# Optimization experiments

Hardware: AMD Instinct MI355X
Metric: run time of the kernel (lower is better)

## Reference

```python
import jax, jax.numpy as jnp
import numpy as np

VEC_DIM = 128   # D (also the per-head dim in this module)
HEADS = 8
PATCH = 4
WIN = 7
N_BATCH = 4
H_IMG = 448
W_IMG = 448


def _relative_index():
    # Swin-style relative position index, computed statically (matches torch code
    # which uses torch.meshgrid with default 'ij' indexing).
    coords = np.stack(np.meshgrid(np.arange(WIN), np.arange(WIN), indexing='ij'))  # [2,W,W]
    flat = coords.reshape(2, -1)                      # [2, W*W]
    rel = flat[:, :, None] - flat[:, None, :]         # [2, p, p]
    rel = rel.transpose(1, 2, 0).astype(np.int64)     # [p, p, 2]
    rel[:, :, 0] += WIN - 1
    rel[:, :, 1] += WIN - 1
    rel[:, :, 1] *= 2 * WIN - 1
    return rel.sum(-1)                                # [p, p], values in [0, (2W-1)^2)

REL_IDX = jnp.asarray(_relative_index())


def setup_inputs() -> dict:
    key = jax.random.key(0)
    ks = jax.random.split(key, 8)
    P = (H_IMG // PATCH) * (W_IMG // PATCH)  # 12544
    D, H = VEC_DIM, HEADS
    s = 0.02
    return {
        'x': jax.random.normal(ks[0], (N_BATCH, D, P), jnp.float32),
        'Wq': jax.random.normal(ks[1], (H * D, D), jnp.float32) * s,
        'bq': jnp.zeros((H * D,), jnp.float32),
        'Wk': jax.random.normal(ks[2], (H * D, D), jnp.float32) * s,
        'bk': jnp.zeros((H * D,), jnp.float32),
        'Wv': jax.random.normal(ks[3], (H * D, D), jnp.float32) * s,
        'bv': jnp.zeros((H * D,), jnp.float32),
        'Wo': jax.random.normal(ks[4], (D, H * D), jnp.float32) * s,
        'bo': jnp.zeros((D,), jnp.float32),
        'pos_code': jax.random.normal(ks[5], ((2 * WIN - 1) ** 2, H), jnp.float32) * s,
        'h': H_IMG,
        'w': W_IMG,
    }


def reference(x, Wq, bq, Wk, bk, Wv, bv, Wo, bo, pos_code, h, w):
    N, D, P = x.shape
    H = HEADS
    ch, cw = h // PATCH, w // PATCH
    nh, nw = ch // WIN, cw // WIN            # windows per axis
    p = WIN * WIN                            # tokens per window

    def emb(W, b):
        # pointwise Conv1d: [N,D,P] -> [N,H*D,P] -> [N,H,D,P]
        return (jnp.einsum('od,ndp->nop', W, x) + b[None, :, None]).reshape(N, H, D, P)

    def partition(e):
        # [N,H,D,P] -> [N,H,win_num,D,p]
        e = e.reshape(N, H, D, nh, WIN, nw, WIN)
        return e.transpose(0, 1, 3, 5, 2, 4, 6).reshape(N, H, nh * nw, D, p)

    q = partition(emb(Wq, bq))
    k = partition(emb(Wk, bk))
    v = partition(emb(Wv, bv))

    # attn[n,h,w,i,j] = sum_d k[n,h,w,d,i] * q[n,h,w,d,j], scaled
    attn = jnp.einsum('nhwdi,nhwdj->nhwij', k, q) / (D ** 0.5)
    bias = pos_code[REL_IDX].transpose(2, 0, 1)          # [H, p, p]
    attn = attn + bias[None, :, None, :, :]
    weights = jax.nn.softmax(attn, axis=3)               # softmax over key index i

    # out[n,h,w,d,j] = sum_i v[n,h,w,d,i] * weights[n,h,w,i,j]
    out = jnp.einsum('nhwdi,nhwij->nhwdj', v, weights)

    # window merge: [N,H,win_num,D,p] -> [N,H*D,P]
    out = out.reshape(N, H, nh, nw, D, WIN, WIN)
    out = out.transpose(0, 1, 4, 2, 5, 3, 6).reshape(N, H * D, P)

    return jnp.einsum('od,ndp->nop', Wo, out) + bo[None, :, None]
```

## Files before the change

### kernel.cpp

```cpp
#include <hip/hip_runtime.h>

typedef unsigned short u16;
typedef unsigned int u32;
typedef __attribute__((ext_vector_type(8))) short bf16x8;
typedef __attribute__((ext_vector_type(4))) float f32x4;
typedef __attribute__((ext_vector_type(2))) unsigned int u32x2;

#define NBATCH 4
#define DDIM   128
#define NHEAD  8
#define PTOT   12544
#define CWID   112
#define NTOK   49
#define PSTR   68

#define OFF_TS 0
#define OFF_US 6272
#define OFF_PL 14464
#define OFF_PC 17796
#define OFF_MF 19148
#define OFF_CS 21196
#define LDS_TOT 22220

#define WS_WC   131072
#define WS_F32  262144

__device__ __forceinline__ int swz128(int row, int col) {
    return row * 128 + ((((col >> 3) ^ row) & 15) << 3) + (col & 7);
}
__device__ __forceinline__ int swz64(int row, int col) {
    return row * 64 + ((((col >> 3) ^ row) & 7) << 3) + (col & 7);
}
__device__ __forceinline__ float bf2f(u16 u) {
    union { u32 i; float f; } x; x.i = ((u32)u) << 16; return x.f;
}
__device__ __forceinline__ u16 f2bf(float f) {
    union { float f; u32 u; } v; v.f = f;
    return (u16)((v.u + 0x7fffu + ((v.u >> 16) & 1u)) >> 16);
}

__global__ void __launch_bounds__(256) prep(
    const float* __restrict__ Wq, const float* __restrict__ Wk,
    const float* __restrict__ Wv, const float* __restrict__ Wo,
    const float* __restrict__ bq, const float* __restrict__ bk,
    const float* __restrict__ bv, u16* __restrict__ ws)
{
    __shared__ u16 lm[32768];
    const int tid = threadIdx.x;
    const int b = blockIdx.x;
    const bool isG = (b >= 8);
    const int h = b & 7;
    float* fb = (float*)(ws + WS_F32);

    if (!isG) {
        for (int idx = tid; idx < 16384; idx += 256) {
            const int dd = idx >> 7, dh = idx & 127;
            lm[swz128(dd, dh)] = f2bf(Wo[dd * 1024 + h * 128 + dh]);
        }
        for (int idx = tid; idx < 16384; idx += 256) {
            const int dh = idx >> 7, d = idx & 127;
            lm[16384 + swz128(d, dh)] = f2bf(Wv[(h * 128 + dh) * 128 + d]);
        }
        if (tid < 128) {
            float s = 0.f;
            for (int dh = 0; dh < 128; ++dh)
                s += Wo[tid * 1024 + h * 128 + dh] * bv[h * 128 + dh];
            fb[h * 128 + tid] = s;
        }
    } else {
        for (int idx = tid; idx < 16384; idx += 256) {
            const int dh = idx >> 7, d = idx & 127;
            lm[swz128(d, dh)] = f2bf(Wk[(h * 128 + dh) * 128 + d]);
        }
        for (int idx = tid; idx < 16384; idx += 256) {
            const int dh = idx >> 7, dp = idx & 127;
            lm[16384 + swz128(dp, dh)] = f2bf(Wq[(h * 128 + dh) * 128 + dp]);
        }
        if (tid < 128) {
            float r = 0.f, m = 0.f;
            for (int dh = 0; dh < 128; ++dh) {
                r += bk[h * 128 + dh] * Wq[(h * 128 + dh) * 128 + tid];
                m += Wk[(h * 128 + dh) * 128 + tid] * bq[h * 128 + dh];
            }
            fb[1024 + h * 128 + tid] = r;
            fb[2048 + h * 128 + tid] = m;
        }
        if (tid == 0) {
            float s = 0.f;
            for (int dh = 0; dh < 128; ++dh) s += bk[h * 128 + dh] * bq[h * 128 + dh];
            fb[3072 + h] = s;
        }
    }
    __syncthreads();

    const int w = tid >> 6, lane = tid & 63, quad = lane >> 4, lid = lane & 15;
    const f32x4 z4 = {0.f, 0.f, 0.f, 0.f};
    u16* dst = ws + (isG ? 0 : WS_WC) + h * 16384;
    #pragma unroll
    for (int mtl = 0; mtl < 2; ++mtl) {
        const int mt = 2 * w + mtl;
        bf16x8 A[4];
        #pragma unroll
        for (int kt = 0; kt < 4; ++kt)
            A[kt] = *(const bf16x8*)(lm + swz128(mt * 16 + lid, kt * 32 + quad * 8));
        #pragma unroll
        for (int nt = 0; nt < 8; ++nt) {
            f32x4 acc = z4;
            #pragma unroll
            for (int kt = 0; kt < 4; ++kt) {
                bf16x8 B = *(const bf16x8*)(lm + 16384 + swz128(nt * 16 + lid, kt * 32 + quad * 8));
                acc = __builtin_amdgcn_mfma_f32_16x16x32_bf16(A[kt], B, acc, 0, 0, 0);
            }
            #pragma unroll
            for (int r = 0; r < 4; ++r) {
                const int row = mt * 16 + quad * 4 + r, col = nt * 16 + lid;
                if (isG) dst[col * 128 + row] = f2bf(acc[r]);
                else     dst[row * 128 + col] = f2bf(acc[r]);
            }
        }
    }
}

__global__ void __launch_bounds__(256, 2)
winattn(const float* __restrict__ xg, const u16* __restrict__ ws,
        const float* __restrict__ bo, const float* __restrict__ posf,
        float* __restrict__ out)
{
    __shared__ u16 sm[LDS_TOT];
    u16* xw = sm;
    u16* ts = sm + OFF_TS;
    u16* us = sm + OFF_US;
    u16* pl = sm + OFF_PL;
    u16* pc = sm + OFF_PC;
    float* Mf = (float*)(sm + OFF_MF);
    float* cs = (float*)(sm + OFF_CS);

    const int tid  = threadIdx.x;
    const int w    = tid >> 6;
    const int lane = tid & 63;
    const int quad = lane >> 4;
    const int lid  = lane & 15;
    const int bx   = blockIdx.x;
    const int n    = bx >> 8;
    const int win  = bx & 255;
    const int pbase = (win >> 4) * 7 * CWID + (win & 15) * 7;

    const bf16x8 zf = {0,0,0,0,0,0,0,0};
    const f32x4  z4 = {0.f,0.f,0.f,0.f};

    const u16* Gt  = ws;
    const u16* Wcw = ws + WS_WC;
    const float* fb  = (const float*)(ws + WS_F32);
    const float* bcv = fb;
    const float* rP  = fb + 1024;
    const float* MP  = fb + 2048;
    const float* sP  = fb + 3072;

    for (int i = tid; i < 169 * NHEAD; i += 256) pc[i] = f2bf(posf[i]);
    for (int i = tid; i < 1024; i += 256) Mf[i] = MP[i];
    const float* xn = xg + n * DDIM * PTOT;
    for (int idx = tid; idx < DDIM * NTOK; idx += 256) {
        int d = idx / NTOK;
        int t = idx - d * NTOK;
        int a = t / 7, b = t - a * 7;
        xw[swz128(t, d)] = f2bf(xn[d * PTOT + pbase + a * CWID + b]);
    }
    __syncthreads();

    bf16x8 xfrag[4][4];
    #pragma unroll
    for (int mt = 0; mt < 4; ++mt)
        #pragma unroll
        for (int kt = 0; kt < 4; ++kt)
            xfrag[mt][kt] = (mt * 16 + lid < NTOK)
                ? *(const bf16x8*)(xw + swz128(mt * 16 + lid, kt * 32 + quad * 8)) : zf;
    const int j = 16 * w + lid;
    bf16x8 xq[4];
    #pragma unroll
    for (int kt = 0; kt < 4; ++kt)
        xq[kt] = (j < NTOK)
            ? *(const bf16x8*)(xw + swz128(j, kt * 32 + quad * 8)) : zf;

    for (int hh = w; hh < NHEAD; hh += 4) {
        const float sh = sP[hh];
        #pragma unroll
        for (int mt = 0; mt < 4; ++mt) {
            float c = 0.f;
            #pragma unroll
            for (int kt = 0; kt < 4; ++kt)
                #pragma unroll
                for (int jj = 0; jj < 8; ++jj)
                    c += bf2f((u16)xfrag[mt][kt][jj]) * Mf[hh * 128 + kt * 32 + quad * 8 + jj];
            c += __shfl_xor(c, 16);
            c += __shfl_xor(c, 32);
            if (quad == 0) cs[hh * 64 + mt * 16 + lid] = c + sh;
        }
    }
    __syncthreads();

    f32x4 outacc[8];
    #pragma unroll
    for (int nt = 0; nt < 8; ++nt) outacc[nt] = z4;

    const int jc = j < NTOK ? j : NTOK - 1;

    for (int h = 0; h < NHEAD; ++h) {
        #pragma unroll
        for (int ntl = 0; ntl < 2; ++ntl) {
            const int nt = 2 * w + ntl;
            bf16x8 B[4];
            #pragma unroll
            for (int kt = 0; kt < 4; ++kt)
                B[kt] = *(const bf16x8*)(Gt + h * 16384 + (nt * 16 + lid) * 128 + kt * 32 + quad * 8);
            const float rbias = rP[h * 128 + nt * 16 + lid];
            #pragma unroll
            for (int mt = 0; mt < 4; ++mt) {
                f32x4 acc = z4;
                #pragma unroll
                for (int kt = 0; kt < 4; ++kt)
                    acc = __builtin_amdgcn_mfma_f32_16x16x32_bf16(xfrag[mt][kt], B[kt], acc, 0, 0, 0);
                #pragma unroll
                for (int r = 0; r < 4; ++r) {
                    const int t = mt * 16 + quad * 4 + r;
                    if (t < NTOK)
                        ts[swz128(t, nt * 16 + lid)] = f2bf(acc[r] + rbias);
                }
            }
        }
        #pragma unroll
        for (int mtl = 0; mtl < 2; ++mtl) {
            const int mt = 2 * w + mtl;
            bf16x8 A[4];
            #pragma unroll
            for (int kt = 0; kt < 4; ++kt)
                A[kt] = *(const bf16x8*)(Wcw + h * 16384 + (mt * 16 + lid) * 128 + kt * 32 + quad * 8);
            float bias[4];
            #pragma unroll
            for (int r = 0; r < 4; ++r)
                bias[r] = bcv[h * 128 + mt * 16 + quad * 4 + r];
            #pragma unroll
            for (int nt = 0; nt < 4; ++nt) {
                f32x4 acc = z4;
                #pragma unroll
                for (int kt = 0; kt < 4; ++kt)
                    acc = __builtin_amdgcn_mfma_f32_16x16x32_bf16(A[kt], xfrag[nt][kt], acc, 0, 0, 0);
                #pragma unroll
                for (int r = 0; r < 4; ++r)
                    us[swz64(mt * 16 + quad * 4 + r, nt * 16 + lid)] = f2bf(acc[r] + bias[r]);
            }
        }
        __syncthreads();

        f32x4 S[4];
        #pragma unroll
        for (int mt = 0; mt < 4; ++mt) {
            S[mt] = z4;
            #pragma unroll
            for (int kt = 0; kt < 4; ++kt) {
                bf16x8 A = *(const bf16x8*)(ts + swz128(mt * 16 + lid, kt * 32 + quad * 8));
                S[mt] = __builtin_amdgcn_mfma_f32_16x16x32_bf16(A, xq[kt], S[mt], 0, 0, 0);
            }
        }
        const int aj = jc / 7, bj = jc - aj * 7;
        float sv[4][4];
        float mx = -3.0e38f;
        #pragma unroll
        for (int mt = 0; mt < 4; ++mt)
            #pragma unroll
            for (int r = 0; r < 4; ++r) {
                const int ii = mt * 16 + quad * 4 + r;
                float vvv;
                if (ii < NTOK) {
                    const int ai = ii / 7, bi = ii - ai * 7;
                    const int rel = (ai - aj + 6) + 13 * (bi - bj + 6);
                    vvv = (S[mt][r] + cs[h * 64 + ii]) * 0.08838834764831845f + bf2f(pc[rel * NHEAD + h]);
                } else {
                    vvv = -3.0e38f;
                }
                sv[mt][r] = vvv;
                mx = fmaxf(mx, vvv);
            }
        mx = fmaxf(mx, __shfl_xor(mx, 16));
        mx = fmaxf(mx, __shfl_xor(mx, 32));
        float ssum = 0.f;
        #pragma unroll
        for (int mt = 0; mt < 4; ++mt)
            #pragma unroll
            for (int r = 0; r < 4; ++r) {
                const float e = __expf(sv[mt][r] - mx);
                sv[mt][r] = e;
                ssum += e;
            }
        ssum += __shfl_xor(ssum, 16);
        ssum += __shfl_xor(ssum, 32);
        const float inv = 1.0f / ssum;
        if (j < NTOK) {
            #pragma unroll
            for (int mt = 0; mt < 4; ++mt) {
                union { u16 s[4]; u32x2 u; } pk;
                #pragma unroll
                for (int r = 0; r < 4; ++r) pk.s[r] = f2bf(sv[mt][r] * inv);
                *(u32x2*)(pl + j * PSTR + mt * 16 + quad * 4) = pk.u;
            }
        }
        __threadfence_block();

        #pragma unroll
        for (int kt = 0; kt < 2; ++kt) {
            union { bf16x8 v; u32 u[4]; } Af;
            #pragma unroll
            for (int q2 = 0; q2 < 4; ++q2)
                Af.u[q2] = *(const u32*)(pl + jc * PSTR + kt * 32 + quad * 8 + 2 * q2);
            #pragma unroll
            for (int nt = 0; nt < 8; ++nt) {
                bf16x8 Bu = *(const bf16x8*)(us + swz64(nt * 16 + lid, kt * 32 + quad * 8));
                outacc[nt] = __builtin_amdgcn_mfma_f32_16x16x32_bf16(Af.v, Bu, outacc[nt], 0, 0, 0);
            }
        }
        __syncthreads();
    }

    float* outp = out + n * DDIM * PTOT;
    #pragma unroll
    for (int nt = 0; nt < 8; ++nt) {
        const int dd = nt * 16 + lid;
        const float bov = bo[dd];
        #pragma unroll
        for (int r = 0; r < 4; ++r) {
            const int jj = 16 * w + quad * 4 + r;
            if (jj < NTOK) {
                const int a = jj / 7, b = jj - a * 7;
                outp[dd * PTOT + pbase + a * CWID + b] = outacc[nt][r] + bov;
            }
        }
    }
}

extern "C" void kernel_launch(void* const* d_in, const int* in_sizes, int n_in,
                              void* d_out, int out_size, void* d_ws, size_t ws_size,
                              hipStream_t stream) {
    (void)in_sizes; (void)n_in; (void)ws_size; (void)out_size;
    prep<<<16, 256, 0, stream>>>((const float*)d_in[1], (const float*)d_in[3],
                                 (const float*)d_in[5], (const float*)d_in[7],
                                 (const float*)d_in[2], (const float*)d_in[4],
                                 (const float*)d_in[6], (u16*)d_ws);
    winattn<<<NBATCH * 256, 256, 0, stream>>>(
        (const float*)d_in[0], (const u16*)d_ws,
        (const float*)d_in[8], (const float*)d_in[9], (float*)d_out);
}
```

Measured before the change: 259.0 us.

## Double-buffer per-head LDS tiles to drop trailing barrier, pack bf16 stores

Per-head T and U tiles are now written into alternating LDS buffers, which lets the end-of-head __syncthreads be removed so one barrier per head iteration is enough. The GEMMs are reoriented so each lane writes four consecutive bf16 values as one packed 8-byte store, using hardware float2-to-bf16 conversion. The softmax scale is folded into the precomputed G matrix and bias vectors, the position table is kept in fp32 in LDS, and the M bias vector is read from global memory instead of being staged in LDS. LDS use per block grows to about 80KB, which may limit occupancy to two blocks per CU. Relying on double buffering alone for the write-after-read hazard is a correctness risk.

```diff
diff --git a/kernel.cpp b/kernel.cpp
--- a/kernel.cpp
+++ b/kernel.cpp
@@ -1,4 +1,5 @@
 #include <hip/hip_runtime.h>
+#include <hip/hip_bf16.h>
 
 typedef unsigned short u16;
 typedef unsigned int u32;
@@ -13,24 +14,24 @@
 #define CWID   112
 #define NTOK   49
 #define PSTR   68
-
-#define OFF_TS 0
-#define OFF_US 6272
-#define OFF_PL 14464
-#define OFF_PC 17796
-#define OFF_MF 19148
-#define OFF_CS 21196
-#define LDS_TOT 22220
-
-#define WS_WC   131072
-#define WS_F32  262144
-
-__device__ __forceinline__ int swz128(int row, int col) {
-    return row * 128 + ((((col >> 3) ^ row) & 15) << 3) + (col & 7);
-}
-__device__ __forceinline__ int swz64(int row, int col) {
-    return row * 64 + ((((col >> 3) ^ row) & 7) << 3) + (col & 7);
-}
+#define SCALE  0.08838834764831845f
+
+#define BUFSZ   14464
+#undef BUFSZ
+#define BUFSZ   16384
+#define OFF_US  8192
+#define OFF_PL  32768
+#define OFF_PCF 36100
+#define OFF_MF  38804
+#define OFF_CS  40852
+#define LDS_TOT 41876
+
+#undef OFF_MF
+#undef OFF_CS
+#undef LDS_TOT
+#define OFF_CS  38804
+#define LDS_TOT 39828
+
 __device__ __forceinline__ float bf2f(u16 u) {
     union { u32 i; float f; } x; x.i = ((u32)u) << 16; return x.f;
 }
@@ -38,6 +39,18 @@
     union { float f; u32 u; } v; v.f = f;
     return (u16)((v.u + 0x7fffu + ((v.u >> 16) & 1u)) >> 16);
 }
+__device__ __forceinline__ u32 pk2(float a, float b) {
+    union { __hip_bfloat162 h; u32 u; } c;
+    float2 t; t.x = a; t.y = b;
+    c.h = __float22bfloat162_rn(t);
+    return c.u;
+}
+__device__ __forceinline__ int swz128(int row, int col) {
+    return row * 128 + ((((col >> 3) ^ (row & 15)) & 15) << 3) + (col & 7);
+}
+
+#define WS_WC   131072
+#define WS_F32  262144
 
 __global__ void __launch_bounds__(256) prep(
     const float* __restrict__ Wq, const float* __restrict__ Wk,
@@ -82,13 +95,13 @@
                 r += bk[h * 128 + dh] * Wq[(h * 128 + dh) * 128 + tid];
                 m += Wk[(h * 128 + dh) * 128 + tid] * bq[h * 128 + dh];
             }
-            fb[1024 + h * 128 + tid] = r;
-            fb[2048 + h * 128 + tid] = m;
+            fb[1024 + h * 128 + tid] = r * SCALE;
+            fb[2048 + h * 128 + tid] = m * SCALE;
         }
         if (tid == 0) {
             float s = 0.f;
             for (int dh = 0; dh < 128; ++dh) s += bk[h * 128 + dh] * bq[h * 128 + dh];
-            fb[3072 + h] = s;
+            fb[3072 + h] = s * SCALE;
         }
     }
     __syncthreads();
@@ -96,6 +109,7 @@
     const int w = tid >> 6, lane = tid & 63, quad = lane >> 4, lid = lane & 15;
     const f32x4 z4 = {0.f, 0.f, 0.f, 0.f};
     u16* dst = ws + (isG ? 0 : WS_WC) + h * 16384;
+    const float gs = isG ? SCALE : 1.0f;
     #pragma unroll
     for (int mtl = 0; mtl < 2; ++mtl) {
         const int mt = 2 * w + mtl;
@@ -114,7 +128,7 @@
             #pragma unroll
             for (int r = 0; r < 4; ++r) {
                 const int row = mt * 16 + quad * 4 + r, col = nt * 16 + lid;
-                if (isG) dst[col * 128 + row] = f2bf(acc[r]);
+                if (isG) dst[col * 128 + row] = f2bf(acc[r] * gs);
                 else     dst[row * 128 + col] = f2bf(acc[r]);
             }
         }
@@ -126,14 +140,11 @@
         const float* __restrict__ bo, const float* __restrict__ posf,
         float* __restrict__ out)
 {
-    __shared__ u16 sm[LDS_TOT];
-    u16* xw = sm;
-    u16* ts = sm + OFF_TS;
-    u16* us = sm + OFF_US;
-    u16* pl = sm + OFF_PL;
-    u16* pc = sm + OFF_PC;
-    float* Mf = (float*)(sm + OFF_MF);
-    float* cs = (float*)(sm + OFF_CS);
+    __shared__ __align__(16) u16 sm[LDS_TOT];
+    u16* xw  = sm;
+    u16* pl  = sm + OFF_PL;
+    float* pcf = (float*)(sm + OFF_PCF);
+    float* cs  = (float*)(sm + OFF_CS);
 
     const int tid  = threadIdx.x;
     const int w    = tid >> 6;
@@ -156,8 +167,7 @@
     const float* MP  = fb + 2048;
     const float* sP  = fb + 3072;
 
-    for (int i = tid; i < 169 * NHEAD; i += 256) pc[i] = f2bf(posf[i]);
-    for (int i = tid; i < 1024; i += 256) Mf[i] = MP[i];
+    for (int i = tid; i < 169 * NHEAD; i += 256) pcf[i] = posf[i];
     const float* xn = xg + n * DDIM * PTOT;
     for (int idx = tid; idx < DDIM * NTOK; idx += 256) {
         int d = idx / NTOK;
@@ -190,7 +200,7 @@
             for (int kt = 0; kt < 4; ++kt)
                 #pragma unroll
                 for (int jj = 0; jj < 8; ++jj)
-                    c += bf2f((u16)xfrag[mt][kt][jj]) * Mf[hh * 128 + kt * 32 + quad * 8 + jj];
+                    c += bf2f((u16)xfrag[mt][kt][jj]) * MP[hh * 128 + kt * 32 + quad * 8 + jj];
             c += __shfl_xor(c, 16);
             c += __shfl_xor(c, 32);
             if (quad == 0) cs[hh * 64 + mt * 16 + lid] = c + sh;
@@ -205,48 +215,51 @@
     const int jc = j < NTOK ? j : NTOK - 1;
 
     for (int h = 0; h < NHEAD; ++h) {
+        u16* tsb = sm + (h & 1) * BUFSZ;
+        u16* usb = tsb + OFF_US;
+
+        #pragma unroll
+        for (int mtl = 0; mtl < 2; ++mtl) {
+            const int mt = 2 * w + mtl;
+            bf16x8 A[4];
+            #pragma unroll
+            for (int kt = 0; kt < 4; ++kt)
+                A[kt] = *(const bf16x8*)(Gt + h * 16384 + (mt * 16 + lid) * 128 + kt * 32 + quad * 8);
+            const f32x4 rb = *(const f32x4*)(rP + h * 128 + mt * 16 + quad * 4);
+            const int dpb = mt * 16 + quad * 4;
+            #pragma unroll
+            for (int nt = 0; nt < 4; ++nt) {
+                f32x4 acc = z4;
+                #pragma unroll
+                for (int kt = 0; kt < 4; ++kt)
+                    acc = __builtin_amdgcn_mfma_f32_16x16x32_bf16(A[kt], xfrag[nt][kt], acc, 0, 0, 0);
+                const int i = nt * 16 + lid;
+                u32x2 pkv;
+                pkv.x = pk2(acc[0] + rb[0], acc[1] + rb[1]);
+                pkv.y = pk2(acc[2] + rb[2], acc[3] + rb[3]);
+                *(u32x2*)(tsb + i * 128 + ((((dpb >> 3) ^ (i & 15)) & 15) << 3) + (dpb & 7)) = pkv;
+            }
+        }
         #pragma unroll
         for (int ntl = 0; ntl < 2; ++ntl) {
             const int nt = 2 * w + ntl;
             bf16x8 B[4];
             #pragma unroll
             for (int kt = 0; kt < 4; ++kt)
-                B[kt] = *(const bf16x8*)(Gt + h * 16384 + (nt * 16 + lid) * 128 + kt * 32 + quad * 8);
-            const float rbias = rP[h * 128 + nt * 16 + lid];
+                B[kt] = *(const bf16x8*)(Wcw + h * 16384 + (nt * 16 + lid) * 128 + kt * 32 + quad * 8);
+            const int dd = nt * 16 + lid;
+            const float bb = bcv[h * 128 + dd];
             #pragma unroll
             for (int mt = 0; mt < 4; ++mt) {
                 f32x4 acc = z4;
                 #pragma unroll
                 for (int kt = 0; kt < 4; ++kt)
                     acc = __builtin_amdgcn_mfma_f32_16x16x32_bf16(xfrag[mt][kt], B[kt], acc, 0, 0, 0);
-                #pragma unroll
-                for (int r = 0; r < 4; ++r) {
-                    const int t = mt * 16 + quad * 4 + r;
-                    if (t < NTOK)
-                        ts[swz128(t, nt * 16 + lid)] = f2bf(acc[r] + rbias);
-                }
-            }
-        }
-        #pragma unroll
-        for (int mtl = 0; mtl < 2; ++mtl) {
-            const int mt = 2 * w + mtl;
-            bf16x8 A[4];
-            #pragma unroll
-            for (int kt = 0; kt < 4; ++kt)
-                A[kt] = *(const bf16x8*)(Wcw + h * 16384 + (mt * 16 + lid) * 128 + kt * 32 + quad * 8);
-            float bias[4];
-            #pragma unroll
-            for (int r = 0; r < 4; ++r)
-                bias[r] = bcv[h * 128 + mt * 16 + quad * 4 + r];
-            #pragma unroll
-            for (int nt = 0; nt < 4; ++nt) {
-                f32x4 acc = z4;
-                #pragma unroll
-                for (int kt = 0; kt < 4; ++kt)
-                    acc = __builtin_amdgcn_mfma_f32_16x16x32_bf16(A[kt], xfrag[nt][kt], acc, 0, 0, 0);
-                #pragma unroll
-                for (int r = 0; r < 4; ++r)
-                    us[swz64(mt * 16 + quad * 4 + r, nt * 16 + lid)] = f2bf(acc[r] + bias[r]);
+                const int ib = mt * 16 + quad * 4;
+                u32x2 pkv;
+                pkv.x = pk2(acc[0] + bb, acc[1] + bb);
+                pkv.y = pk2(acc[2] + bb, acc[3] + bb);
+                *(u32x2*)(usb + dd * 64 + ((((ib >> 3) ^ (dd & 7)) & 7) << 3) + (ib & 7)) = pkv;
             }
         }
         __syncthreads();
@@ -257,7 +270,7 @@
             S[mt] = z4;
             #pragma unroll
             for (int kt = 0; kt < 4; ++kt) {
-                bf16x8 A = *(const bf16x8*)(ts + swz128(mt * 16 + lid, kt * 32 + quad * 8));
+                bf16x8 A = *(const bf16x8*)(tsb + (mt * 16 + lid) * 128 + ((((kt * 4 + quad) ^ lid) & 15) << 3));
                 S[mt] = __builtin_amdgcn_mfma_f32_16x16x32_bf16(A, xq[kt], S[mt], 0, 0, 0);
             }
         }
@@ -273,7 +286,7 @@
                 if (ii < NTOK) {
                     const int ai = ii / 7, bi = ii - ai * 7;
                     const int rel = (ai - aj + 6) + 13 * (bi - bj + 6);
-                    vvv = (S[mt][r] + cs[h * 64 + ii]) * 0.08838834764831845f + bf2f(pc[rel * NHEAD + h]);
+                    vvv = S[mt][r] + cs[h * 64 + ii] + pcf[rel * NHEAD + h];
                 } else {
                     vvv = -3.0e38f;
                 }
@@ -297,10 +310,10 @@
         if (j < NTOK) {
             #pragma unroll
             for (int mt = 0; mt < 4; ++mt) {
-                union { u16 s[4]; u32x2 u; } pk;
-                #pragma unroll
-                for (int r = 0; r < 4; ++r) pk.s[r] = f2bf(sv[mt][r] * inv);
-                *(u32x2*)(pl + j * PSTR + mt * 16 + quad * 4) = pk.u;
+                u32x2 pkv;
+                pkv.x = pk2(sv[mt][0] * inv, sv[mt][1] * inv);
+                pkv.y = pk2(sv[mt][2] * inv, sv[mt][3] * inv);
+                *(u32x2*)(pl + j * PSTR + mt * 16 + quad * 4) = pkv;
             }
         }
         __threadfence_block();
@@ -313,11 +326,11 @@
                 Af.u[q2] = *(const u32*)(pl + jc * PSTR + kt * 32 + quad * 8 + 2 * q2);
             #pragma unroll
             for (int nt = 0; nt < 8; ++nt) {
-                bf16x8 Bu = *(const bf16x8*)(us + swz64(nt * 16 + lid, kt * 32 + quad * 8));
+                const int dd = nt * 16 + lid;
+                bf16x8 Bu = *(const bf16x8*)(usb + dd * 64 + ((((kt * 4 + quad) ^ (dd & 7)) & 7) << 3));
                 outacc[nt] = __builtin_amdgcn_mfma_f32_16x16x32_bf16(Af.v, Bu, outacc[nt], 0, 0, 0);
             }
         }
-        __syncthreads();
     }
 
     float* outp = out + n * DDIM * PTOT;
```

Result: faster. 236.0 us (-8.9%).
